# Kernel tuning notes

Measured on AMD Instinct MI355X. Metric: run time of the kernel, lower is better.

The kernel has to match this reference:

```python
import jax, jax.numpy as jnp
import numpy as np

B, T, D, H, O = 512, 512, 256, 200, 1


def setup_inputs() -> dict:
    key = jax.random.key(0)
    ks = jax.random.split(key, 7)
    s = 1.0 / np.sqrt(H)  # PyTorch LSTM init scale
    x = jax.random.normal(ks[0], (B, T, D), dtype=jnp.float32)
    W_ih = jax.random.uniform(ks[1], (4 * H, D), jnp.float32, -s, s)
    W_hh = jax.random.uniform(ks[2], (4 * H, H), jnp.float32, -s, s)
    b_ih = jax.random.uniform(ks[3], (4 * H,), jnp.float32, -s, s)
    b_hh = jax.random.uniform(ks[4], (4 * H,), jnp.float32, -s, s)
    so = 1.0 / np.sqrt(H * T)
    W_out = jax.random.uniform(ks[5], (O, H * T), jnp.float32, -so, so)
    b_out = jax.random.uniform(ks[6], (O,), jnp.float32, -so, so)
    return {"input_seq": x, "W_ih": W_ih, "W_hh": W_hh, "b_ih": b_ih,
            "b_hh": b_hh, "W_out": W_out, "b_out": b_out}


def _lstm(x, W_ih, W_hh, b_ih, b_hh):
    # Precompute input contribution for all timesteps: [B,T,4H] -> [T,B,4H]
    pre = jnp.einsum('btd,gd->btg', x, W_ih) + b_ih + b_hh
    pre = jnp.transpose(pre, (1, 0, 2))
    h0 = jnp.zeros((x.shape[0], H), x.dtype)
    c0 = jnp.zeros((x.shape[0], H), x.dtype)

    def step(carry, pt):
        h, c = carry
        gates = pt + h @ W_hh.T  # [B,4H]
        i, f, g, o = jnp.split(gates, 4, axis=-1)  # PyTorch gate order i,f,g,o
        i = jax.nn.sigmoid(i)
        f = jax.nn.sigmoid(f)
        g = jnp.tanh(g)
        o = jax.nn.sigmoid(o)
        c_new = f * c + i * g
        h_new = o * jnp.tanh(c_new)
        return (h_new, c_new), h_new

    _, outs = jax.lax.scan(step, (h0, c0), pre)  # outs: [T,B,H]
    return jnp.transpose(outs, (1, 0, 2))  # [B,T,H]


def reference(input_seq, W_ih, W_hh, b_ih, b_hh, W_out, b_out):
    all_outs = _lstm(input_seq, W_ih, W_hh, b_ih, b_hh)  # [B,T,H]
    flat = all_outs.reshape(all_outs.shape[0], -1)  # [B, T*H]
    return flat @ W_out.T + b_out  # [B, O]
```

## Files before the change

### kernel.cpp

```cpp
#include <hip/hip_runtime.h>
#include <hip/hip_bf16.h>

#define B_SZ 512
#define T_SZ 512
#define D_SZ 256
#define H_SZ 200
#define G4   800
#define NSUB 50
#define BS   8
#define WROW 800

typedef __attribute__((ext_vector_type(8))) short short8;
typedef __attribute__((ext_vector_type(4))) short short4v;
typedef __attribute__((ext_vector_type(4))) float f32x4;

__device__ __forceinline__ unsigned short f2bf(float x) {
    unsigned u = __builtin_bit_cast(unsigned, x);
    unsigned r = (u + 0x7FFFu + ((u >> 16) & 1u)) >> 16;
    return (unsigned short)r;
}
__device__ __forceinline__ float sigm(float v) { return 1.f / (1.f + __expf(-v)); }

__device__ __forceinline__ void gl_lds16(const void* g, void* l) {
    __builtin_amdgcn_global_load_lds(
        (const __attribute__((address_space(1))) unsigned int*)g,
        (__attribute__((address_space(3))) unsigned int*)l, 16, 0, 0);
}

__global__ __launch_bounds__(256)
void cvt_bf16(const float* __restrict__ src, unsigned short* __restrict__ dst, int n4)
{
    int i = blockIdx.x * 256 + threadIdx.x;
    const int stride = gridDim.x * 256;
    for (; i < n4; i += stride) {
        float4 v = ((const float4*)src)[i];
        unsigned a = (unsigned)f2bf(v.x) | ((unsigned)f2bf(v.y) << 16);
        unsigned b = (unsigned)f2bf(v.z) | ((unsigned)f2bf(v.w) << 16);
        ((uint2*)dst)[i] = make_uint2(a, b);
    }
}

__global__ __launch_bounds__(256)
void cvt_w_perm(const float* __restrict__ Wih, unsigned short* __restrict__ dst)
{
    int i = blockIdx.x * 256 + threadIdx.x;
    if (i >= G4 * (D_SZ / 4)) return;
    const int r = i >> 6, ch = i & 63;
    const int p = (r & 3) * H_SZ + (r >> 2);
    float4 v = ((const float4*)(Wih + (size_t)p * D_SZ))[ch];
    unsigned a = (unsigned)f2bf(v.x) | ((unsigned)f2bf(v.y) << 16);
    unsigned b = (unsigned)f2bf(v.z) | ((unsigned)f2bf(v.w) << 16);
    ((uint2*)dst)[i] = make_uint2(a, b);
}

__global__ __launch_bounds__(256)
void prep(const float* __restrict__ bih, const float* __restrict__ bhh,
          const float* __restrict__ Wout, float* __restrict__ bsum,
          float* __restrict__ wpad)
{
    const int i = blockIdx.x * 256 + threadIdx.x;
    if (i < G4) {
        const int p = (i & 3) * H_SZ + (i >> 2);
        bsum[i] = bih[p] + bhh[p];
    }
    if (i < T_SZ * H_SZ + 256)
        wpad[i] = (i < T_SZ * H_SZ) ? Wout[i] : 0.f;
}

__global__ __launch_bounds__(512)
void pre_gemm(const unsigned short* __restrict__ xbf,
              const unsigned short* __restrict__ wbf,
              const float* __restrict__ bs,
              unsigned short* __restrict__ pre, int t0)
{
    const int tt = blockIdx.x;
    const int t  = t0 + tt;
    const int b0 = blockIdx.y * 128;
    const int g0 = blockIdx.z * 256;

    __shared__ unsigned short Al[256 * 32];
    __shared__ unsigned short Bl[128 * 32];

    const int tid  = threadIdx.x;
    const int wv   = tid >> 6;
    const int lane = tid & 63;
    const int col  = lane & 15, q = lane >> 4;
    const int wm   = wv >> 1;
    const int wn   = wv & 1;

    f32x4 acc[4][4];
    #pragma unroll
    for (int i = 0; i < 4; ++i)
        #pragma unroll
        for (int j = 0; j < 4; ++j) acc[i][j] = (f32x4)0.f;

    const int arow_l = lane >> 2;
    const int akoff  = (lane & 3) * 8;

    for (int kc = 0; kc < 8; ++kc) {
        const int d0 = kc * 32;
        if (kc) __syncthreads();
        #pragma unroll
        for (int j = 0; j < 2; ++j) {
            int g = g0 + wv * 32 + j * 16 + arow_l;
            if (g > G4 - 1) g = G4 - 1;
            gl_lds16(wbf + (size_t)g * D_SZ + d0 + akoff,
                     (void*)(Al + (wv * 32 + j * 16) * 32));
        }
        {
            const int brow = b0 + wv * 16 + arow_l;
            gl_lds16(xbf + ((size_t)brow * T_SZ + t) * D_SZ + d0 + akoff,
                     (void*)(Bl + (wv * 16) * 32));
        }
        __syncthreads();

        short8 af[4], bv[4];
        #pragma unroll
        for (int s = 0; s < 4; ++s)
            af[s] = *(const short8*)&Al[(wm * 64 + s * 16 + col) * 32 + q * 8];
        #pragma unroll
        for (int s = 0; s < 4; ++s)
            bv[s] = *(const short8*)&Bl[(wn * 64 + s * 16 + col) * 32 + q * 8];
        #pragma unroll
        for (int gs = 0; gs < 4; ++gs)
            #pragma unroll
            for (int bsi = 0; bsi < 4; ++bsi)
                acc[gs][bsi] = __builtin_amdgcn_mfma_f32_16x16x32_bf16(af[gs], bv[bsi], acc[gs][bsi], 0, 0, 0);
    }

    #pragma unroll
    for (int gs = 0; gs < 4; ++gs) {
        const int S = blockIdx.z * 16 + wm * 4 + gs;
        if (S < NSUB) {
            const int gq = S * 16 + q * 4;
            const float4 bi = *(const float4*)&bs[gq];
            #pragma unroll
            for (int bsi = 0; bsi < 4; ++bsi) {
                f32x4 a = acc[gs][bsi];
                unsigned lo = (unsigned)f2bf(a[0] + bi.x) |
                              ((unsigned)f2bf(a[1] + bi.y) << 16);
                unsigned hi = (unsigned)f2bf(a[2] + bi.z) |
                              ((unsigned)f2bf(a[3] + bi.w) << 16);
                const size_t idx = (((size_t)tt * NSUB + S) * 4 + q) * 512 +
                                   (b0 + wn * 64 + bsi * 16 + col);
                ((uint2*)pre)[idx] = make_uint2(lo, hi);
            }
        }
    }
}

__global__ __launch_bounds__(512, 2)
void lstm_rec(const unsigned short* __restrict__ pre,
              const float* __restrict__ Whh,
              const float* __restrict__ wpad,
              const float* __restrict__ bout,
              float* __restrict__ state,
              float* __restrict__ out,
              int t0, int C_T)
{
    const int bk = blockIdx.x;
    const int cidx = (bk >> 3) + (bk & 7) * 32;
    const int b0 = cidx * 2;

    const int tid = threadIdx.x, lane = tid & 63, wv = tid >> 6;
    const int col = lane & 15, q = lane >> 4;

    __shared__ __align__(16) unsigned short preS[2 * BS * 1600];
    __shared__ __align__(16) short hT[1600];
    __shared__ __align__(16) float woutS[2 * BS * 256];
    __shared__ float redbuf[16];

    const int tbase = (wv < 2) ? wv * 7 : 14 + (wv - 2) * 6;

    int pofs[7], tjv[7];
    #pragma unroll
    for (int j = 0; j < 7; ++j) {
        const int tr = tbase + j;
        const int tj = tr > 49 ? 49 : tr;
        tjv[j] = tj;
        pofs[j] = (tj * 4 + q) * 8 + (col >> 3) * 4;
    }
    const int c7 = col & 7;
    const int jsel = (c7 < 7) ? c7 : 6;
    const bool valid = (wv < 2) ? (c7 < 7) : (c7 < 6);
    const int bsel = col >> 3;
    const int usel = tjv[jsel] * 4 + q;
    const int hw_base = valid ? (bsel * 256 + usel) : (1024 + lane);
    const int rbase = bsel * 256;

    short8 aw[7][6];
#if __has_builtin(__builtin_amdgcn_mfma_f32_16x16x16bf16_1k)
    short4v aw6[7];
#else
    short8 aw6[7];
#endif
    #pragma unroll
    for (int j = 0; j < 7; ++j) {
        const int gp = tjv[j] * 16 + col;
        const float* wr = Whh + (size_t)((gp & 3) * H_SZ + (gp >> 2)) * H_SZ;
        #pragma unroll
        for (int kc = 0; kc < 6; ++kc) {
            const int k = kc * 32 + q * 8;
            float4 f0 = *(const float4*)(wr + k);
            float4 f1 = *(const float4*)(wr + k + 4);
            short8 s;
            s[0] = (short)f2bf(f0.x); s[1] = (short)f2bf(f0.y);
            s[2] = (short)f2bf(f0.z); s[3] = (short)f2bf(f0.w);
            s[4] = (short)f2bf(f1.x); s[5] = (short)f2bf(f1.y);
            s[6] = (short)f2bf(f1.z); s[7] = (short)f2bf(f1.w);
            aw[j][kc] = s;
        }
#if __has_builtin(__builtin_amdgcn_mfma_f32_16x16x16bf16_1k)
        short4v t4 = (short4v)0;
        if (q < 2) {
            float4 f = *(const float4*)(wr + 192 + q * 4);
            t4[0] = (short)f2bf(f.x); t4[1] = (short)f2bf(f.y);
            t4[2] = (short)f2bf(f.z); t4[3] = (short)f2bf(f.w);
        }
        aw6[j] = t4;
#else
        short8 t8 = (short8)0;
        if (q == 0) {
            float4 f0 = *(const float4*)(wr + 192);
            float4 f1 = *(const float4*)(wr + 196);
            t8[0] = (short)f2bf(f0.x); t8[1] = (short)f2bf(f0.y);
            t8[2] = (short)f2bf(f0.z); t8[3] = (short)f2bf(f0.w);
            t8[4] = (short)f2bf(f1.x); t8[5] = (short)f2bf(f1.y);
            t8[6] = (short)f2bf(f1.z); t8[7] = (short)f2bf(f1.w);
        }
        aw6[j] = t8;
#endif
    }

    float* h_st  = state;
    float* c_st  = state + (size_t)B_SZ * H_SZ;
    float* oa_st = state + (size_t)2 * B_SZ * H_SZ;

    for (int i = tid; i < 1600; i += 512) {
        short v = 0;
        if (t0 > 0 && i < 512) {
            const int r = i >> 8, u = i & 255;
            if (u < H_SZ) v = (short)f2bf(h_st[(size_t)(b0 + r) * H_SZ + u]);
        }
        hT[i] = v;
    }

    float c_v = 0.f, oa_v = 0.f;
    if (t0 > 0 && valid) {
        c_v  = c_st [(size_t)(b0 + bsel) * H_SZ + usel];
        oa_v = oa_st[(size_t)(b0 + bsel) * H_SZ + usel];
    }

    const int nblk = C_T / BS;
    const char* preb = (const char*)pre;

    {
        const char* src = preb + ((size_t)wv * 200) * 4096 + (size_t)b0 * 8;
        unsigned short* dst = preS + (0 * BS + wv) * 1600;
        gl_lds16(src + (size_t)lane * 4096,         dst);
        gl_lds16(src + (size_t)(lane + 64) * 4096,  dst + 512);
        gl_lds16(src + (size_t)(lane + 128) * 4096, dst + 1024);
        gl_lds16(src + (size_t)(lane + 136) * 4096, dst + 1088);
        gl_lds16((const char*)wpad + (size_t)(t0 + wv) * WROW + lane * 16,
                 (void*)(woutS + wv * 256));
    }
    __syncthreads();

    for (int blk = 0; blk < nblk; ++blk) {
        const int bn = blk & 1;
        {
            const int nb = (blk + 1 < nblk) ? blk + 1 : blk;
            const char* src = preb + ((size_t)(nb * BS + wv) * 200) * 4096 + (size_t)b0 * 8;
            unsigned short* dst = preS + ((bn ^ 1) * BS + wv) * 1600;
            gl_lds16(src + (size_t)lane * 4096,         dst);
            gl_lds16(src + (size_t)(lane + 64) * 4096,  dst + 512);
            gl_lds16(src + (size_t)(lane + 128) * 4096, dst + 1024);
            gl_lds16(src + (size_t)(lane + 136) * 4096, dst + 1088);
            gl_lds16((const char*)wpad + (size_t)(t0 + nb * BS + wv) * WROW + lane * 16,
                     (void*)(woutS + ((bn ^ 1) * BS + wv) * 256));
        }
        const unsigned short* psb = preS + bn * (BS * 1600);

        uint2 pr[7];
        #pragma unroll
        for (int j = 0; j < 7; ++j)
            pr[j] = *(const uint2*)(psb + pofs[j]);
        float wout_c = woutS[(bn * BS) * 256 + usel];

        #pragma unroll
        for (int s = 0; s < BS; ++s) {
            const int tc = blk * BS + s;
            const short* hrow = hT + ((tc & 1) << 9) + rbase;

            f32x4 acc[7];
            #pragma unroll
            for (int j = 0; j < 7; ++j) {
                f32x4 a;
                a[0] = __builtin_bit_cast(float, pr[j].x << 16);
                a[1] = __builtin_bit_cast(float, pr[j].x & 0xFFFF0000u);
                a[2] = __builtin_bit_cast(float, pr[j].y << 16);
                a[3] = __builtin_bit_cast(float, pr[j].y & 0xFFFF0000u);
                acc[j] = a;
            }
            #pragma unroll
            for (int kc = 0; kc < 6; ++kc) {
                const short8 bf = *(const short8*)(hrow + kc * 32 + q * 8);
                #pragma unroll
                for (int j = 0; j < 7; ++j)
                    acc[j] = __builtin_amdgcn_mfma_f32_16x16x32_bf16(aw[j][kc], bf, acc[j], 0, 0, 0);
            }
#if __has_builtin(__builtin_amdgcn_mfma_f32_16x16x16bf16_1k)
            {
                const short4v bt = *(const short4v*)(hrow + 192 + q * 4);
                #pragma unroll
                for (int j = 0; j < 7; ++j)
                    acc[j] = __builtin_amdgcn_mfma_f32_16x16x16bf16_1k(aw6[j], bt, acc[j], 0, 0, 0);
            }
#else
            {
                const short8 bt = *(const short8*)(hrow + 192 + q * 8);
                #pragma unroll
                for (int j = 0; j < 7; ++j)
                    acc[j] = __builtin_amdgcn_mfma_f32_16x16x32_bf16(aw6[j], bt, acc[j], 0, 0, 0);
            }
#endif
            f32x4 sel = acc[0];
            #pragma unroll
            for (int j = 1; j < 7; ++j)
                if (jsel == j) sel = acc[j];

            const float gi = sigm(sel[0]);
            const float gf = sigm(sel[1]);
            const float gg = 2.f * sigm(2.f * sel[2]) - 1.f;
            const float go = sigm(sel[3]);
            const float cn = gf * c_v + gi * gg;
            c_v = cn;
            const float hv = go * (2.f * sigm(2.f * cn) - 1.f);
            oa_v += hv * wout_c;
            hT[hw_base + (((tc + 1) & 1) << 9)] = (short)f2bf(hv);
            if (t0 + C_T < T_SZ && tc == C_T - 1 && valid)
                h_st[(size_t)(b0 + bsel) * H_SZ + usel] = hv;

            if (s < BS - 1) {
                #pragma unroll
                for (int j = 0; j < 7; ++j)
                    pr[j] = *(const uint2*)(psb + (s + 1) * 1600 + pofs[j]);
                wout_c = woutS[(bn * BS + s + 1) * 256 + usel];
                asm volatile("s_waitcnt lgkmcnt(0)\n\ts_barrier" ::: "memory");
            } else {
                __syncthreads();
            }
        }
    }

    if (t0 + C_T >= T_SZ) {
        float v = valid ? oa_v : 0.f;
        v += __shfl_xor(v, 1);
        v += __shfl_xor(v, 2);
        v += __shfl_xor(v, 4);
        v += __shfl_xor(v, 16);
        v += __shfl_xor(v, 32);
        if (lane == 0) redbuf[wv * 2]     = v;
        if (lane == 8) redbuf[wv * 2 + 1] = v;
        __syncthreads();
        if (tid < 2) {
            float r = bout[0];
            #pragma unroll
            for (int w = 0; w < 8; ++w) r += redbuf[w * 2 + tid];
            out[b0 + tid] = r;
        }
    } else if (valid) {
        c_st [(size_t)(b0 + bsel) * H_SZ + usel] = c_v;
        oa_st[(size_t)(b0 + bsel) * H_SZ + usel] = oa_v;
    }
}

extern "C" void kernel_launch(void* const* d_in, const int* in_sizes, int n_in,
                              void* d_out, int out_size, void* d_ws, size_t ws_size,
                              hipStream_t stream)
{
    const float* x    = (const float*)d_in[0];
    const float* Wih  = (const float*)d_in[1];
    const float* Whh  = (const float*)d_in[2];
    const float* bih  = (const float*)d_in[3];
    const float* bhh  = (const float*)d_in[4];
    const float* Wout = (const float*)d_in[5];
    const float* bout = (const float*)d_in[6];
    float* out = (float*)d_out;

    char* ws = (char*)d_ws;
    float* state = (float*)ws;
    size_t off = (size_t)3 * B_SZ * H_SZ * sizeof(float);
    float* bsum = (float*)(ws + off);
    off += (size_t)G4 * sizeof(float);
    float* wpad = (float*)(ws + off);
    off += (size_t)(T_SZ * H_SZ + 256) * sizeof(float);
    unsigned short* xbf = (unsigned short*)(ws + off);
    off += (size_t)B_SZ * T_SZ * D_SZ * 2;
    unsigned short* wbf = (unsigned short*)(ws + off);
    off += (size_t)G4 * D_SZ * 2;
    unsigned short* pre = (unsigned short*)(ws + off);

    const size_t per_t = (size_t)NSUB * 4 * 512 * 4 * 2;
    int ct = 512;
    while (ct > BS && off + (size_t)ct * per_t > ws_size) ct >>= 1;

    cvt_bf16<<<dim3(2048), dim3(256), 0, stream>>>(x, xbf, B_SZ * T_SZ * D_SZ / 4);
    cvt_w_perm<<<dim3(200), dim3(256), 0, stream>>>(Wih, wbf);
    prep<<<dim3(402), dim3(256), 0, stream>>>(bih, bhh, Wout, bsum, wpad);

    for (int t0 = 0; t0 < T_SZ; t0 += ct) {
        pre_gemm<<<dim3(ct, 4, 4), dim3(512), 0, stream>>>(
            xbf, wbf, bsum, pre, t0);
        lstm_rec<<<dim3(256), dim3(512), 0, stream>>>(
            pre, Whh, wpad, bout, state, out, t0, ct);
    }
}
```

Baseline: 1.667 ms.

## Shrink pre-GEMM gate tiles and skip padded MFMA tiles in recurrence

The input-projection GEMM now uses 256-thread blocks covering 128 gate rows each, launched over 7 gate blocks instead of 4. This cuts the padded work beyond 800 gates and gives more blocks for occupancy. In the recurrent kernel the 50 gate tiles are reassigned so every wave owns 6 tiles and only two waves take a seventh. A templated step then issues 6 or 7 MFMA chains instead of always 7, and raises wave priority around the MFMA block. The cost is a divergent code path per wave, and the extra tile lands on two waves, which may become the critical path.

```diff
diff --git a/kernel.cpp b/kernel.cpp
--- a/kernel.cpp
+++ b/kernel.cpp
@@ -14,6 +14,14 @@
 typedef __attribute__((ext_vector_type(4))) short short4v;
 typedef __attribute__((ext_vector_type(4))) float f32x4;
 
+#if __has_builtin(__builtin_amdgcn_mfma_f32_16x16x16bf16_1k)
+#define HAS_1K 1
+typedef short4v aw6_t;
+#else
+#define HAS_1K 0
+typedef short8 aw6_t;
+#endif
+
 __device__ __forceinline__ unsigned short f2bf(float x) {
     unsigned u = __builtin_bit_cast(unsigned, x);
     unsigned r = (u + 0x7FFFu + ((u >> 16) & 1u)) >> 16;
@@ -67,7 +75,7 @@
         wpad[i] = (i < T_SZ * H_SZ) ? Wout[i] : 0.f;
 }
 
-__global__ __launch_bounds__(512)
+__global__ __launch_bounds__(256)
 void pre_gemm(const unsigned short* __restrict__ xbf,
               const unsigned short* __restrict__ wbf,
               const float* __restrict__ bs,
@@ -76,9 +84,9 @@
     const int tt = blockIdx.x;
     const int t  = t0 + tt;
     const int b0 = blockIdx.y * 128;
-    const int g0 = blockIdx.z * 256;
-
-    __shared__ unsigned short Al[256 * 32];
+    const int g0 = blockIdx.z * 128;
+
+    __shared__ unsigned short Al[128 * 32];
     __shared__ unsigned short Bl[128 * 32];
 
     const int tid  = threadIdx.x;
@@ -107,10 +115,11 @@
             gl_lds16(wbf + (size_t)g * D_SZ + d0 + akoff,
                      (void*)(Al + (wv * 32 + j * 16) * 32));
         }
-        {
-            const int brow = b0 + wv * 16 + arow_l;
+        #pragma unroll
+        for (int j = 0; j < 2; ++j) {
+            const int brow = b0 + wv * 32 + j * 16 + arow_l;
             gl_lds16(xbf + ((size_t)brow * T_SZ + t) * D_SZ + d0 + akoff,
-                     (void*)(Bl + (wv * 16) * 32));
+                     (void*)(Bl + (wv * 32 + j * 16) * 32));
         }
         __syncthreads();
 
@@ -130,7 +139,7 @@
 
     #pragma unroll
     for (int gs = 0; gs < 4; ++gs) {
-        const int S = blockIdx.z * 16 + wm * 4 + gs;
+        const int S = blockIdx.z * 8 + wm * 4 + gs;
         if (S < NSUB) {
             const int gq = S * 16 + q * 4;
             const float4 bi = *(const float4*)&bs[gq];
@@ -149,6 +158,52 @@
     }
 }
 
+template<int NT>
+__device__ __forceinline__ f32x4 lstm_step(
+    const short8 (&aw)[7][6], const aw6_t (&aw6)[7],
+    const uint2 (&pr)[7], const short* hrow, int jsel, int q)
+{
+    f32x4 acc[NT];
+    #pragma unroll
+    for (int j = 0; j < NT; ++j) {
+        f32x4 a;
+        a[0] = __builtin_bit_cast(float, pr[j].x << 16);
+        a[1] = __builtin_bit_cast(float, pr[j].x & 0xFFFF0000u);
+        a[2] = __builtin_bit_cast(float, pr[j].y << 16);
+        a[3] = __builtin_bit_cast(float, pr[j].y & 0xFFFF0000u);
+        acc[j] = a;
+    }
+    __builtin_amdgcn_s_setprio(1);
+    #pragma unroll
+    for (int kc = 0; kc < 6; ++kc) {
+        const short8 bf = *(const short8*)(hrow + kc * 32 + q * 8);
+        #pragma unroll
+        for (int j = 0; j < NT; ++j)
+            acc[j] = __builtin_amdgcn_mfma_f32_16x16x32_bf16(aw[j][kc], bf, acc[j], 0, 0, 0);
+    }
+#if HAS_1K
+    {
+        const short4v bt = *(const short4v*)(hrow + 192 + q * 4);
+        #pragma unroll
+        for (int j = 0; j < NT; ++j)
+            acc[j] = __builtin_amdgcn_mfma_f32_16x16x16bf16_1k(aw6[j], bt, acc[j], 0, 0, 0);
+    }
+#else
+    {
+        const short8 bt = *(const short8*)(hrow + 192 + q * 8);
+        #pragma unroll
+        for (int j = 0; j < NT; ++j)
+            acc[j] = __builtin_amdgcn_mfma_f32_16x16x32_bf16(aw6[j], bt, acc[j], 0, 0, 0);
+    }
+#endif
+    __builtin_amdgcn_s_setprio(0);
+    f32x4 sel = acc[0];
+    #pragma unroll
+    for (int j = 1; j < NT; ++j)
+        if (jsel == j) sel = acc[j];
+    return sel;
+}
+
 __global__ __launch_bounds__(512, 2)
 void lstm_rec(const unsigned short* __restrict__ pre,
               const float* __restrict__ Whh,
@@ -170,33 +225,26 @@
     __shared__ __align__(16) float woutS[2 * BS * 256];
     __shared__ float redbuf[16];
 
-    const int tbase = (wv < 2) ? wv * 7 : 14 + (wv - 2) * 6;
-
-    int pofs[7], tjv[7];
-    #pragma unroll
-    for (int j = 0; j < 7; ++j) {
-        const int tr = tbase + j;
-        const int tj = tr > 49 ? 49 : tr;
-        tjv[j] = tj;
-        pofs[j] = (tj * 4 + q) * 8 + (col >> 3) * 4;
-    }
     const int c7 = col & 7;
-    const int jsel = (c7 < 7) ? c7 : 6;
-    const bool valid = (wv < 2) ? (c7 < 7) : (c7 < 6);
     const int bsel = col >> 3;
-    const int usel = tjv[jsel] * 4 + q;
+    const int rbase = bsel * 256;
+
+    const int jsel = (c7 < 6) ? c7 : ((c7 == 6 && wv < 2) ? 6 : 0);
+    const bool valid = (c7 < 6) || (c7 == 6 && wv < 2);
+    const int otile = (jsel < 6) ? (wv * 6 + jsel) : (48 + wv);
+    const int usel = otile * 4 + q;
     const int hw_base = valid ? (bsel * 256 + usel) : (1024 + lane);
-    const int rbase = bsel * 256;
+
+    int pofs[7];
+    #pragma unroll
+    for (int j = 0; j < 6; ++j)
+        pofs[j] = ((wv * 6 + j) * 4 + q) * 8 + bsel * 4;
+    pofs[6] = ((48 + (wv & 1)) * 4 + q) * 8 + bsel * 4;
 
     short8 aw[7][6];
-#if __has_builtin(__builtin_amdgcn_mfma_f32_16x16x16bf16_1k)
-    short4v aw6[7];
-#else
-    short8 aw6[7];
-#endif
-    #pragma unroll
-    for (int j = 0; j < 7; ++j) {
-        const int gp = tjv[j] * 16 + col;
+    aw6_t aw6[7];
+    auto ld_aw = [&](int j, int tile) {
+        const int gp = tile * 16 + col;
         const float* wr = Whh + (size_t)((gp & 3) * H_SZ + (gp >> 2)) * H_SZ;
         #pragma unroll
         for (int kc = 0; kc < 6; ++kc) {
@@ -210,7 +258,7 @@
             s[6] = (short)f2bf(f1.z); s[7] = (short)f2bf(f1.w);
             aw[j][kc] = s;
         }
-#if __has_builtin(__builtin_amdgcn_mfma_f32_16x16x16bf16_1k)
+#if HAS_1K
         short4v t4 = (short4v)0;
         if (q < 2) {
             float4 f = *(const float4*)(wr + 192 + q * 4);
@@ -230,7 +278,10 @@
         }
         aw6[j] = t8;
 #endif
-    }
+    };
+    #pragma unroll
+    for (int j = 0; j < 6; ++j) ld_aw(j, wv * 6 + j);
+    if (wv < 2) ld_aw(6, 48 + wv);
 
     float* h_st  = state;
     float* c_st  = state + (size_t)B_SZ * H_SZ;
@@ -292,42 +343,9 @@
             const int tc = blk * BS + s;
             const short* hrow = hT + ((tc & 1) << 9) + rbase;
 
-            f32x4 acc[7];
-            #pragma unroll
-            for (int j = 0; j < 7; ++j) {
-                f32x4 a;
-                a[0] = __builtin_bit_cast(float, pr[j].x << 16);
-                a[1] = __builtin_bit_cast(float, pr[j].x & 0xFFFF0000u);
-                a[2] = __builtin_bit_cast(float, pr[j].y << 16);
-                a[3] = __builtin_bit_cast(float, pr[j].y & 0xFFFF0000u);
-                acc[j] = a;
-            }
-            #pragma unroll
-            for (int kc = 0; kc < 6; ++kc) {
-                const short8 bf = *(const short8*)(hrow + kc * 32 + q * 8);
-                #pragma unroll
-                for (int j = 0; j < 7; ++j)
-                    acc[j] = __builtin_amdgcn_mfma_f32_16x16x32_bf16(aw[j][kc], bf, acc[j], 0, 0, 0);
-            }
-#if __has_builtin(__builtin_amdgcn_mfma_f32_16x16x16bf16_1k)
-            {
-                const short4v bt = *(const short4v*)(hrow + 192 + q * 4);
-                #pragma unroll
-                for (int j = 0; j < 7; ++j)
-                    acc[j] = __builtin_amdgcn_mfma_f32_16x16x16bf16_1k(aw6[j], bt, acc[j], 0, 0, 0);
-            }
-#else
-            {
-                const short8 bt = *(const short8*)(hrow + 192 + q * 8);
-                #pragma unroll
-                for (int j = 0; j < 7; ++j)
-                    acc[j] = __builtin_amdgcn_mfma_f32_16x16x32_bf16(aw6[j], bt, acc[j], 0, 0, 0);
-            }
-#endif
-            f32x4 sel = acc[0];
-            #pragma unroll
-            for (int j = 1; j < 7; ++j)
-                if (jsel == j) sel = acc[j];
+            f32x4 sel;
+            if (wv < 2) sel = lstm_step<7>(aw, aw6, pr, hrow, jsel, q);
+            else        sel = lstm_step<6>(aw, aw6, pr, hrow, jsel, q);
 
             const float gi = sigm(sel[0]);
             const float gf = sigm(sel[1]);
@@ -410,7 +428,7 @@
     prep<<<dim3(402), dim3(256), 0, stream>>>(bih, bhh, Wout, bsum, wpad);
 
     for (int t0 = 0; t0 < T_SZ; t0 += ct) {
-        pre_gemm<<<dim3(ct, 4, 4), dim3(512), 0, stream>>>(
+        pre_gemm<<<dim3(ct, 4, 7), dim3(256), 0, stream>>>(
             xbf, wbf, bsum, pre, t0);
         lstm_rec<<<dim3(256), dim3(512), 0, stream>>>(
             pre, Whh, wpad, bout, state, out, t0, ct);
```

After: 1.619 ms. 2.9% less time.
